# Kernel optimization log

Hardware: AMD Instinct MI355X
Metric: run time of the kernel (lower is better)

The kernel has to match this reference:

```python
import jax, jax.numpy as jnp
import numpy as np

N_EMBD = 2048
N_HEAD = 32
N_KV_HEADS = 8
HEAD_DIM = 64
N_REP = N_HEAD // N_KV_HEADS
MAX_SEQ_LEN = 4096
ROPE_THETA = 10000.0


def _precompute_freqs_cis(dim, end, theta=ROPE_THETA):
    freqs = 1.0 / theta ** (jnp.arange(0, dim, 2)[: dim // 2].astype(jnp.float32) / dim)
    t = jnp.arange(end, dtype=jnp.float32)
    freqs = jnp.outer(t, freqs)  # (end, dim//2)
    return jnp.cos(freqs), jnp.sin(freqs)


def setup_inputs() -> dict:
    key = jax.random.key(0)
    ks = jax.random.split(key, 5)
    B, S = 2, 2048
    x = jax.random.normal(ks[0], (B, S, N_EMBD), dtype=jnp.float32)
    # torch Linear(in, out, bias=False): y = x @ W.T, W is (out, in). We store (in, out).
    sc = 1.0 / np.sqrt(N_EMBD)
    wq = jax.random.normal(ks[1], (N_EMBD, N_EMBD), dtype=jnp.float32) * sc
    wk = jax.random.normal(ks[2], (N_EMBD, N_KV_HEADS * HEAD_DIM), dtype=jnp.float32) * sc
    wv = jax.random.normal(ks[3], (N_EMBD, N_KV_HEADS * HEAD_DIM), dtype=jnp.float32) * sc
    wo = jax.random.normal(ks[4], (N_EMBD, N_EMBD), dtype=jnp.float32) * sc
    freqs_cos, freqs_sin = _precompute_freqs_cis(HEAD_DIM, MAX_SEQ_LEN)
    return {"x": x, "wq": wq, "wk": wk, "wv": wv, "wo": wo,
            "freqs_cos": freqs_cos, "freqs_sin": freqs_sin}


def _apply_rotary(t, cos, sin):
    # t: (B, S, H, HD); interleaved real/imag pairs along last dim.
    shp = t.shape
    t2 = t.reshape(*shp[:-1], HEAD_DIM // 2, 2)
    r, i = t2[..., 0], t2[..., 1]
    out_r = r * cos - i * sin
    out_i = r * sin + i * cos
    return jnp.stack([out_r, out_i], axis=-1).reshape(shp)


def reference(x, wq, wk, wv, wo, freqs_cos, freqs_sin):
    B, S, _ = x.shape
    xq = (x @ wq).reshape(B, S, N_HEAD, HEAD_DIM)
    xk = (x @ wk).reshape(B, S, N_KV_HEADS, HEAD_DIM)
    xv = (x @ wv).reshape(B, S, N_KV_HEADS, HEAD_DIM)

    cos = freqs_cos[:S][None, :, None, :]  # (1, S, 1, HD/2)
    sin = freqs_sin[:S][None, :, None, :]
    xq = _apply_rotary(xq, cos, sin)
    xk = _apply_rotary(xk, cos, sin)

    # GQA: repeat KV heads (repeat_interleave along head dim)
    keys = jnp.repeat(xk, N_REP, axis=2)    # (B, S, H, HD)
    values = jnp.repeat(xv, N_REP, axis=2)

    scores = jnp.einsum('bqhd,bkhd->bhqk', xq, keys) / np.sqrt(HEAD_DIM)
    causal = jnp.tril(jnp.ones((S, S), dtype=bool))
    scores = jnp.where(causal, scores, -jnp.inf)
    probs = jax.nn.softmax(scores.astype(jnp.float32), axis=-1).astype(xq.dtype)
    out = jnp.einsum('bhqk,bkhd->bqhd', probs, values)  # (B, S, H, HD)
    out = out.reshape(B, S, N_EMBD)
    return out @ wo
```

## Files before the change

### kernel.cpp

```cpp
#include <hip/hip_runtime.h>
#include <hip/hip_fp16.h>
#include <stdint.h>

typedef _Float16 f16x8 __attribute__((ext_vector_type(8)));
typedef _Float16 f16x4 __attribute__((ext_vector_type(4)));
typedef _Float16 f16x2 __attribute__((ext_vector_type(2)));
typedef float f32x4 __attribute__((ext_vector_type(4)));
typedef float f32x16 __attribute__((ext_vector_type(16)));

#define B_ 2
#define S_ 2048
#define NE 2048
#define NH 32
#define NKV 8
#define HD 64
#define NTOK (B_ * S_)
#define QKVN 3072

__device__ __forceinline__ f16x2 pk(float a, float b) {
  return __builtin_bit_cast(f16x2, __builtin_amdgcn_cvt_pkrtz(a, b));
}

__device__ __forceinline__ void gld_lds16(void* lds, const void* g) {
  __builtin_amdgcn_global_load_lds(
      (const __attribute__((address_space(1))) void*)g,
      (__attribute__((address_space(3))) void*)lds, 16, 0, 0);
}

__global__ void conv_x_kernel(const float* __restrict__ x,
                              _Float16* __restrict__ xo, int n2) {
  int i = blockIdx.x * 256 + threadIdx.x;
  if (i < n2) {
    float2 v = ((const float2*)x)[i];
    f16x2 h;
    h.x = (_Float16)v.x;
    h.y = (_Float16)v.y;
    ((f16x2*)xo)[i] = h;
  }
}

__global__ void tconv_kernel(const float* __restrict__ src,
                             _Float16* __restrict__ dst,
                             int srcN, int rowoff, int ldd) {
  __shared__ float tile[32][33];
  int n0 = blockIdx.x * 32, k0 = blockIdx.y * 32;
  int tx = threadIdx.x, ty = threadIdx.y;
  for (int i = ty; i < 32; i += 8)
    tile[i][tx] = src[(size_t)(k0 + i) * srcN + n0 + tx];
  __syncthreads();
  for (int i = ty; i < 32; i += 8)
    dst[(size_t)(rowoff + n0 + i) * ldd + k0 + tx] = (_Float16)tile[tx][i];
}

template <int OUT_F32>
__global__ __launch_bounds__(256, 2) void gemm_bt(
    const _Float16* __restrict__ A, const _Float16* __restrict__ Bt,
    void* __restrict__ Cout, int M, int N, int K) {
  __shared__ _Float16 As[128 * 32];
  __shared__ _Float16 Bs[128 * 32];
  const int tid = threadIdx.x;
  const int wave = tid >> 6, lane = tid & 63;
  const int qd = lane >> 4, ln = lane & 15;
  const int m0 = blockIdx.y * 128, n0 = blockIdx.x * 128;
  const int wm = (wave >> 1) * 64, wn = (wave & 1) * 64;

  f32x4 acc[4][4] = {};

  const int srow = (lane >> 2);
  const int scol = (lane & 3) * 8;

  for (int k0 = 0; k0 < K; k0 += 32) {
    __syncthreads();
#pragma unroll
    for (int it = 0; it < 2; ++it) {
      int r = wave * 32 + it * 16 + srow;
      gld_lds16(&As[(wave * 32 + it * 16) * 32],
                A + (size_t)(m0 + r) * K + k0 + scol);
      gld_lds16(&Bs[(wave * 32 + it * 16) * 32],
                Bt + (size_t)(n0 + r) * K + k0 + scol);
    }
    __syncthreads();
    f16x8 a[4], b[4];
#pragma unroll
    for (int mt = 0; mt < 4; ++mt)
      a[mt] = *(const f16x8*)&As[(wm + mt * 16 + ln) * 32 + qd * 8];
#pragma unroll
    for (int nt = 0; nt < 4; ++nt)
      b[nt] = *(const f16x8*)&Bs[(wn + nt * 16 + ln) * 32 + qd * 8];
#pragma unroll
    for (int mt = 0; mt < 4; ++mt)
#pragma unroll
      for (int nt = 0; nt < 4; ++nt)
        acc[mt][nt] =
            __builtin_amdgcn_mfma_f32_16x16x32_f16(a[mt], b[nt], acc[mt][nt], 0, 0, 0);
  }

#pragma unroll
  for (int mt = 0; mt < 4; ++mt) {
    int row = m0 + wm + mt * 16 + qd * 4;
#pragma unroll
    for (int nt = 0; nt < 4; ++nt) {
      int col = n0 + wn + nt * 16 + ln;
#pragma unroll
      for (int r = 0; r < 4; ++r) {
        if (OUT_F32)
          ((float*)Cout)[(size_t)(row + r) * N + col] = acc[mt][nt][r];
        else
          ((_Float16*)Cout)[(size_t)(row + r) * N + col] =
              (_Float16)acc[mt][nt][r];
      }
    }
  }
}

__global__ void rope_scatter_kernel(const _Float16* __restrict__ qkv,
                                    const float* __restrict__ fcos,
                                    const float* __restrict__ fsin,
                                    _Float16* __restrict__ Qb,
                                    _Float16* __restrict__ Kb) {
  const float QSC = 0.125f * 1.44269504088896f;
  int idx = blockIdx.x * 256 + threadIdx.x;
  int t = idx / 1280;
  int col = (idx - t * 1280) * 2;
  int b = t >> 11, s = t & 2047;
  float v0 = (float)qkv[(size_t)t * QKVN + col];
  float v1 = (float)qkv[(size_t)t * QKVN + col + 1];
  _Float16* dst;
  size_t off;
  int d;
  float sc;
  if (col < 2048) {
    int h = col >> 6;
    d = col & 63;
    dst = Qb;
    off = ((size_t)(b * NH + h) * S_ + s) * HD + d;
    sc = QSC;
  } else {
    int cc = col - 2048;
    int h = cc >> 6;
    d = cc & 63;
    dst = Kb;
    off = ((size_t)(b * NKV + h) * S_ + s) * HD + d;
    sc = 1.0f;
  }
  float c = fcos[s * 32 + (d >> 1)], sn = fsin[s * 32 + (d >> 1)];
  f16x2 o;
  o.x = (_Float16)((v0 * c - v1 * sn) * sc);
  o.y = (_Float16)((v0 * sn + v1 * c) * sc);
  *(f16x2*)(dst + off) = o;
}

__global__ void vtrans_kernel(const _Float16* __restrict__ qkv,
                              _Float16* __restrict__ Vtg) {
  __shared__ _Float16 tile[64][65];
  int t0 = blockIdx.x * 64;
  int kv = blockIdx.y, b = blockIdx.z;
  int tid = threadIdx.x;
  for (int slot = tid; slot < 4096; slot += 256) {
    int r = slot >> 6, c = slot & 63;
    tile[r][c] = qkv[(size_t)(b * S_ + t0 + r) * QKVN + 2560 + kv * 64 + c];
  }
  __syncthreads();
  size_t base = ((size_t)(b * NKV + kv) * HD) * S_;
  for (int slot = tid; slot < 4096; slot += 256) {
    int d = slot >> 6, r = slot & 63;
    Vtg[base + (size_t)d * S_ + t0 + r] = tile[r][d];
  }
}

__global__ __launch_bounds__(128, 2) void attn_kernel(
    const _Float16* __restrict__ Qb, const _Float16* __restrict__ Kb,
    const _Float16* __restrict__ Vtg, _Float16* __restrict__ Ob) {
  constexpr float M_SHIFT = 10.0f;
  __shared__ _Float16 Ks[64 * 64];
  __shared__ _Float16 Vs[64 * 64];
  const int tid = threadIdx.x;
  const int wave = tid >> 6, lane = tid & 63;
  const int mrow = lane & 31;
  const bool half = (lane >> 5) != 0;
  const int h = blockIdx.y, b = blockIdx.z;
  const int kvh = h >> 2;

  const _Float16* Qh = Qb + ((size_t)(b * NH + h) * S_) * HD;
  const _Float16* Kh = Kb + ((size_t)(b * NKV + kvh) * S_) * HD;
  const _Float16* Vh = Vtg + ((size_t)(b * NKV + kvh) * HD) * S_;

  const int sr = tid >> 3;
  const int scc = tid & 7;
  const int swz = (scc ^ (sr & 7)) * 8;

#pragma unroll
  for (int pass = 0; pass < 2; ++pass) {
    const int qt = pass ? blockIdx.x : (31 - blockIdx.x);
    const int q0 = qt * 64;
    const int nkt = qt + 1;

    const int qrow = q0 + wave * 32 + mrow;
    f16x8 aq[4];
#pragma unroll
    for (int kk = 0; kk < 4; ++kk)
      aq[kk] = *(const f16x8*)(Qh + (size_t)qrow * HD + kk * 16 +
                               (half ? 8 : 0));

    f32x16 accO[2] = {};
    float lsum = 0.f;

    f16x8 kp[4], vp[4];
#pragma unroll
    for (int i = 0; i < 4; ++i) {
      kp[i] = *(const f16x8*)(Kh + (size_t)(sr + i * 16) * HD + scc * 8);
      vp[i] = *(const f16x8*)(Vh + (size_t)(sr + i * 16) * S_ + scc * 8);
    }
#pragma unroll
    for (int i = 0; i < 4; ++i) {
      *(f16x8*)&Ks[(sr + i * 16) * 64 + swz] = kp[i];
      *(f16x8*)&Vs[(sr + i * 16) * 64 + swz] = vp[i];
    }

    for (int kt = 0; kt < nkt; ++kt) {
      __syncthreads();
      if (kt + 1 < nkt) {
#pragma unroll
        for (int i = 0; i < 4; ++i) {
          kp[i] = *(const f16x8*)(Kh +
                                  (size_t)((kt + 1) * 64 + sr + i * 16) * HD +
                                  scc * 8);
          vp[i] = *(const f16x8*)(Vh + (size_t)(sr + i * 16) * S_ +
                                  (kt + 1) * 64 + scc * 8);
        }
      }

      f32x16 s[2];
#pragma unroll
      for (int nt = 0; nt < 2; ++nt)
#pragma unroll
        for (int r = 0; r < 16; ++r) s[nt][r] = -M_SHIFT;
#pragma unroll
      for (int kk = 0; kk < 4; ++kk) {
        int c = kk * 2 + (half ? 1 : 0);
#pragma unroll
        for (int nt = 0; nt < 2; ++nt) {
          int krow = nt * 32 + mrow;
          f16x8 bk = *(const f16x8*)&Ks[krow * 64 + ((c ^ (krow & 7)) * 8)];
          s[nt] = __builtin_amdgcn_mfma_f32_32x32x16_f16(bk, aq[kk], s[nt],
                                                         0, 0, 0);
        }
      }

      const bool edge = (kt == nkt - 1);
      float pf[2][16];
#pragma unroll
      for (int nt = 0; nt < 2; ++nt)
#pragma unroll
        for (int r = 0; r < 16; ++r) {
          int key = kt * 64 + nt * 32 + (r & 3) + 8 * (r >> 2) +
                    (half ? 4 : 0);
          float p = exp2f(s[nt][r]);
          if (edge && key > qrow) p = 0.f;
          lsum += p;
          pf[nt][r] = p;
        }

      f16x2 P2[2][4][2];
#pragma unroll
      for (int nt = 0; nt < 2; ++nt)
#pragma unroll
        for (int c = 0; c < 4; ++c)
#pragma unroll
          for (int u = 0; u < 2; ++u)
            P2[nt][c][u] = pk(pf[nt][4 * c + 2 * u], pf[nt][4 * c + 2 * u + 1]);

#pragma unroll
      for (int s4 = 0; s4 < 4; ++s4) {
        const int ntp = s4 >> 1;
        const int gA = (2 * s4) & 3, gB = (2 * s4 + 1) & 3;
        f16x2 own0 = half ? P2[ntp][gB][0] : P2[ntp][gA][0];
        f16x2 own1 = half ? P2[ntp][gB][1] : P2[ntp][gA][1];
        f16x2 snd0 = half ? P2[ntp][gA][0] : P2[ntp][gB][0];
        f16x2 snd1 = half ? P2[ntp][gA][1] : P2[ntp][gB][1];
        f16x2 rcv0 = __builtin_bit_cast(
            f16x2, __shfl_xor(__builtin_bit_cast(int, snd0), 32));
        f16x2 rcv1 = __builtin_bit_cast(
            f16x2, __shfl_xor(__builtin_bit_cast(int, snd1), 32));
        union {
          f16x2 h2[4];
          f16x8 h8;
        } bp;
        bp.h2[0] = half ? rcv0 : own0;
        bp.h2[1] = half ? rcv1 : own1;
        bp.h2[2] = half ? own0 : rcv0;
        bp.h2[3] = half ? own1 : rcv1;
        const int c = 2 * s4 + (half ? 1 : 0);
#pragma unroll
        for (int ntd = 0; ntd < 2; ++ntd) {
          int drow = ntd * 32 + mrow;
          f16x8 bv = *(const f16x8*)&Vs[drow * 64 + ((c ^ (drow & 7)) * 8)];
          accO[ntd] = __builtin_amdgcn_mfma_f32_32x32x16_f16(bv, bp.h8,
                                                             accO[ntd], 0, 0, 0);
        }
      }

      __syncthreads();
      if (kt + 1 < nkt) {
#pragma unroll
        for (int i = 0; i < 4; ++i) {
          *(f16x8*)&Ks[(sr + i * 16) * 64 + swz] = kp[i];
          *(f16x8*)&Vs[(sr + i * 16) * 64 + swz] = vp[i];
        }
      }
    }

    float tot = lsum + __shfl_xor(lsum, 32);
    float inv = 1.f / tot;
    size_t base = ((size_t)(b * S_) + qrow) * NE + h * HD;
#pragma unroll
    for (int ntd = 0; ntd < 2; ++ntd)
#pragma unroll
      for (int rq = 0; rq < 4; ++rq) {
        int d0 = ntd * 32 + 8 * rq + (half ? 4 : 0);
        union {
          f16x2 h2[2];
          f16x4 h4;
        } o;
        o.h2[0] = pk(accO[ntd][4 * rq + 0] * inv, accO[ntd][4 * rq + 1] * inv);
        o.h2[1] = pk(accO[ntd][4 * rq + 2] * inv, accO[ntd][4 * rq + 3] * inv);
        *(f16x4*)(Ob + base + d0) = o.h4;
      }
  }
}

extern "C" void kernel_launch(void* const* d_in, const int* in_sizes, int n_in,
                              void* d_out, int out_size, void* d_ws,
                              size_t ws_size, hipStream_t stream) {
  const float* x = (const float*)d_in[0];
  const float* wq = (const float*)d_in[1];
  const float* wk = (const float*)d_in[2];
  const float* wv = (const float*)d_in[3];
  const float* wo = (const float*)d_in[4];
  const float* fcos = (const float*)d_in[5];
  const float* fsin = (const float*)d_in[6];

  char* ws = (char*)d_ws;
  _Float16* xb = (_Float16*)(ws);
  _Float16* wqkv_t = (_Float16*)(ws + 16777216);
  _Float16* wo_t = (_Float16*)(ws + 29360128);
  _Float16* qkv = (_Float16*)(ws + 37748736);
  _Float16* Qb = (_Float16*)(ws + 62914560);
  _Float16* Kb = (_Float16*)(ws + 79691776);
  _Float16* Vb = (_Float16*)(ws + 83886080);
  _Float16* Ob = (_Float16*)(ws + 88080384);

  conv_x_kernel<<<16384, 256, 0, stream>>>(x, xb, (NTOK * NE) / 2);

  dim3 tb(32, 8);
  tconv_kernel<<<dim3(64, 64), tb, 0, stream>>>(wq, wqkv_t, 2048, 0, 2048);
  tconv_kernel<<<dim3(16, 64), tb, 0, stream>>>(wk, wqkv_t, 512, 2048, 2048);
  tconv_kernel<<<dim3(16, 64), tb, 0, stream>>>(wv, wqkv_t, 512, 2560, 2048);
  tconv_kernel<<<dim3(64, 64), tb, 0, stream>>>(wo, wo_t, 2048, 0, 2048);

  gemm_bt<0><<<dim3(QKVN / 128, NTOK / 128), 256, 0, stream>>>(
      xb, wqkv_t, qkv, NTOK, QKVN, NE);

  rope_scatter_kernel<<<(NTOK * 1280) / 256, 256, 0, stream>>>(qkv, fcos, fsin,
                                                               Qb, Kb);
  vtrans_kernel<<<dim3(S_ / 64, NKV, B_), 256, 0, stream>>>(qkv, Vb);

  attn_kernel<<<dim3(16, NH, B_), 128, 0, stream>>>(Qb, Kb, Vb, Ob);

  gemm_bt<1><<<dim3(NE / 128, NTOK / 128), 256, 0, stream>>>(
      Ob, wo_t, d_out, NTOK, NE, NE);
}
```

Measured before the change: 327.2 us.

## Split attention KV loop across two wave pairs and reduce partials in LDS

The attention block grows from 2 to 4 waves. Each pair of waves processes alternate KV tiles using its own K/V LDS buffers, so each pair covers about half the key range for the same 64 query rows. The partial output accumulators and row sums from pair 1 are passed through LDS and added into pair 0, which then normalises and writes the result. This doubles the waves available per query tile to hide latency on the causal loop. In exchange it costs extra LDS, a final cross-pair reduction, and some redundant tile loads when a pair has no valid tile.

```diff
diff --git a/kernel.cpp b/kernel.cpp
--- a/kernel.cpp
+++ b/kernel.cpp
@@ -168,25 +168,33 @@
   }
 }
 
-__global__ __launch_bounds__(128, 2) void attn_kernel(
+__global__ __launch_bounds__(256, 4) void attn_kernel(
     const _Float16* __restrict__ Qb, const _Float16* __restrict__ Kb,
     const _Float16* __restrict__ Vtg, _Float16* __restrict__ Ob) {
   constexpr float M_SHIFT = 10.0f;
-  __shared__ _Float16 Ks[64 * 64];
-  __shared__ _Float16 Vs[64 * 64];
+  __shared__ _Float16 smem[4 * 64 * 64];
+  __shared__ float lsx[128];
   const int tid = threadIdx.x;
-  const int wave = tid >> 6, lane = tid & 63;
+  const int wave = tid >> 6;
+  const int pair = wave >> 1;
+  const int wq = wave & 1;
+  const int lane = tid & 63;
   const int mrow = lane & 31;
   const bool half = (lane >> 5) != 0;
   const int h = blockIdx.y, b = blockIdx.z;
   const int kvh = h >> 2;
 
+  _Float16* Ksp = smem + pair * 8192;
+  _Float16* Vsp = Ksp + 4096;
+  float* cb = (float*)smem;
+
   const _Float16* Qh = Qb + ((size_t)(b * NH + h) * S_) * HD;
   const _Float16* Kh = Kb + ((size_t)(b * NKV + kvh) * S_) * HD;
   const _Float16* Vh = Vtg + ((size_t)(b * NKV + kvh) * HD) * S_;
 
-  const int sr = tid >> 3;
-  const int scc = tid & 7;
+  const int ptid = tid & 127;
+  const int sr = ptid >> 3;
+  const int scc = ptid & 7;
   const int swz = (scc ^ (sr & 7)) * 8;
 
 #pragma unroll
@@ -194,8 +202,9 @@
     const int qt = pass ? blockIdx.x : (31 - blockIdx.x);
     const int q0 = qt * 64;
     const int nkt = qt + 1;
-
-    const int qrow = q0 + wave * 32 + mrow;
+    const int NI = (nkt + 1) >> 1;
+
+    const int qrow = q0 + wq * 32 + mrow;
     f16x8 aq[4];
 #pragma unroll
     for (int kk = 0; kk < 4; ++kk)
@@ -205,127 +214,159 @@
     f32x16 accO[2] = {};
     float lsum = 0.f;
 
+    const int t0 = (pair < nkt) ? pair : (nkt - 1);
     f16x8 kp[4], vp[4];
 #pragma unroll
     for (int i = 0; i < 4; ++i) {
-      kp[i] = *(const f16x8*)(Kh + (size_t)(sr + i * 16) * HD + scc * 8);
-      vp[i] = *(const f16x8*)(Vh + (size_t)(sr + i * 16) * S_ + scc * 8);
+      kp[i] = *(const f16x8*)(Kh + (size_t)(t0 * 64 + sr + i * 16) * HD +
+                              scc * 8);
+      vp[i] = *(const f16x8*)(Vh + (size_t)(sr + i * 16) * S_ + t0 * 64 +
+                              scc * 8);
     }
 #pragma unroll
     for (int i = 0; i < 4; ++i) {
-      *(f16x8*)&Ks[(sr + i * 16) * 64 + swz] = kp[i];
-      *(f16x8*)&Vs[(sr + i * 16) * 64 + swz] = vp[i];
-    }
-
-    for (int kt = 0; kt < nkt; ++kt) {
+      *(f16x8*)&Ksp[(sr + i * 16) * 64 + swz] = kp[i];
+      *(f16x8*)&Vsp[(sr + i * 16) * 64 + swz] = vp[i];
+    }
+
+    for (int it = 0; it < NI; ++it) {
       __syncthreads();
-      if (kt + 1 < nkt) {
+      const int kt = 2 * it + pair;
+      const bool valid = kt < nkt;
+      if (it + 1 < NI) {
+        const int tn0 = 2 * (it + 1) + pair;
+        const int tn = (tn0 < nkt) ? tn0 : (nkt - 1);
 #pragma unroll
         for (int i = 0; i < 4; ++i) {
-          kp[i] = *(const f16x8*)(Kh +
-                                  (size_t)((kt + 1) * 64 + sr + i * 16) * HD +
+          kp[i] = *(const f16x8*)(Kh + (size_t)(tn * 64 + sr + i * 16) * HD +
                                   scc * 8);
-          vp[i] = *(const f16x8*)(Vh + (size_t)(sr + i * 16) * S_ +
-                                  (kt + 1) * 64 + scc * 8);
+          vp[i] = *(const f16x8*)(Vh + (size_t)(sr + i * 16) * S_ + tn * 64 +
+                                  scc * 8);
         }
       }
 
-      f32x16 s[2];
-#pragma unroll
-      for (int nt = 0; nt < 2; ++nt)
-#pragma unroll
-        for (int r = 0; r < 16; ++r) s[nt][r] = -M_SHIFT;
-#pragma unroll
-      for (int kk = 0; kk < 4; ++kk) {
-        int c = kk * 2 + (half ? 1 : 0);
-#pragma unroll
-        for (int nt = 0; nt < 2; ++nt) {
-          int krow = nt * 32 + mrow;
-          f16x8 bk = *(const f16x8*)&Ks[krow * 64 + ((c ^ (krow & 7)) * 8)];
-          s[nt] = __builtin_amdgcn_mfma_f32_32x32x16_f16(bk, aq[kk], s[nt],
-                                                         0, 0, 0);
+      if (valid) {
+        f32x16 s[2];
+#pragma unroll
+        for (int nt = 0; nt < 2; ++nt)
+#pragma unroll
+          for (int r = 0; r < 16; ++r) s[nt][r] = -M_SHIFT;
+#pragma unroll
+        for (int kk = 0; kk < 4; ++kk) {
+          int c = kk * 2 + (half ? 1 : 0);
+#pragma unroll
+          for (int nt = 0; nt < 2; ++nt) {
+            int krow = nt * 32 + mrow;
+            f16x8 bk = *(const f16x8*)&Ksp[krow * 64 + ((c ^ (krow & 7)) * 8)];
+            s[nt] = __builtin_amdgcn_mfma_f32_32x32x16_f16(bk, aq[kk], s[nt],
+                                                           0, 0, 0);
+          }
+        }
+
+        const bool edge = (kt == nkt - 1);
+        float pf[2][16];
+#pragma unroll
+        for (int nt = 0; nt < 2; ++nt)
+#pragma unroll
+          for (int r = 0; r < 16; ++r) {
+            int key = kt * 64 + nt * 32 + (r & 3) + 8 * (r >> 2) +
+                      (half ? 4 : 0);
+            float p = exp2f(s[nt][r]);
+            if (edge && key > qrow) p = 0.f;
+            lsum += p;
+            pf[nt][r] = p;
+          }
+
+        f16x2 P2[2][4][2];
+#pragma unroll
+        for (int nt = 0; nt < 2; ++nt)
+#pragma unroll
+          for (int c = 0; c < 4; ++c)
+#pragma unroll
+            for (int u = 0; u < 2; ++u)
+              P2[nt][c][u] =
+                  pk(pf[nt][4 * c + 2 * u], pf[nt][4 * c + 2 * u + 1]);
+
+#pragma unroll
+        for (int s4 = 0; s4 < 4; ++s4) {
+          const int ntp = s4 >> 1;
+          const int gA = (2 * s4) & 3, gB = (2 * s4 + 1) & 3;
+          f16x2 own0 = half ? P2[ntp][gB][0] : P2[ntp][gA][0];
+          f16x2 own1 = half ? P2[ntp][gB][1] : P2[ntp][gA][1];
+          f16x2 snd0 = half ? P2[ntp][gA][0] : P2[ntp][gB][0];
+          f16x2 snd1 = half ? P2[ntp][gA][1] : P2[ntp][gB][1];
+          f16x2 rcv0 = __builtin_bit_cast(
+              f16x2, __shfl_xor(__builtin_bit_cast(int, snd0), 32));
+          f16x2 rcv1 = __builtin_bit_cast(
+              f16x2, __shfl_xor(__builtin_bit_cast(int, snd1), 32));
+          union {
+            f16x2 h2[4];
+            f16x8 h8;
+          } bp;
+          bp.h2[0] = half ? rcv0 : own0;
+          bp.h2[1] = half ? rcv1 : own1;
+          bp.h2[2] = half ? own0 : rcv0;
+          bp.h2[3] = half ? own1 : rcv1;
+          const int c = 2 * s4 + (half ? 1 : 0);
+#pragma unroll
+          for (int ntd = 0; ntd < 2; ++ntd) {
+            int drow = ntd * 32 + mrow;
+            f16x8 bv = *(const f16x8*)&Vsp[drow * 64 + ((c ^ (drow & 7)) * 8)];
+            accO[ntd] = __builtin_amdgcn_mfma_f32_32x32x16_f16(
+                bv, bp.h8, accO[ntd], 0, 0, 0);
+          }
         }
       }
 
-      const bool edge = (kt == nkt - 1);
-      float pf[2][16];
-#pragma unroll
-      for (int nt = 0; nt < 2; ++nt)
-#pragma unroll
-        for (int r = 0; r < 16; ++r) {
-          int key = kt * 64 + nt * 32 + (r & 3) + 8 * (r >> 2) +
-                    (half ? 4 : 0);
-          float p = exp2f(s[nt][r]);
-          if (edge && key > qrow) p = 0.f;
-          lsum += p;
-          pf[nt][r] = p;
-        }
-
-      f16x2 P2[2][4][2];
-#pragma unroll
-      for (int nt = 0; nt < 2; ++nt)
-#pragma unroll
-        for (int c = 0; c < 4; ++c)
-#pragma unroll
-          for (int u = 0; u < 2; ++u)
-            P2[nt][c][u] = pk(pf[nt][4 * c + 2 * u], pf[nt][4 * c + 2 * u + 1]);
-
-#pragma unroll
-      for (int s4 = 0; s4 < 4; ++s4) {
-        const int ntp = s4 >> 1;
-        const int gA = (2 * s4) & 3, gB = (2 * s4 + 1) & 3;
-        f16x2 own0 = half ? P2[ntp][gB][0] : P2[ntp][gA][0];
-        f16x2 own1 = half ? P2[ntp][gB][1] : P2[ntp][gA][1];
-        f16x2 snd0 = half ? P2[ntp][gA][0] : P2[ntp][gB][0];
-        f16x2 snd1 = half ? P2[ntp][gA][1] : P2[ntp][gB][1];
-        f16x2 rcv0 = __builtin_bit_cast(
-            f16x2, __shfl_xor(__builtin_bit_cast(int, snd0), 32));
-        f16x2 rcv1 = __builtin_bit_cast(
-            f16x2, __shfl_xor(__builtin_bit_cast(int, snd1), 32));
-        union {
-          f16x2 h2[4];
-          f16x8 h8;
-        } bp;
-        bp.h2[0] = half ? rcv0 : own0;
-        bp.h2[1] = half ? rcv1 : own1;
-        bp.h2[2] = half ? own0 : rcv0;
-        bp.h2[3] = half ? own1 : rcv1;
-        const int c = 2 * s4 + (half ? 1 : 0);
-#pragma unroll
-        for (int ntd = 0; ntd < 2; ++ntd) {
-          int drow = ntd * 32 + mrow;
-          f16x8 bv = *(const f16x8*)&Vs[drow * 64 + ((c ^ (drow & 7)) * 8)];
-          accO[ntd] = __builtin_amdgcn_mfma_f32_32x32x16_f16(bv, bp.h8,
-                                                             accO[ntd], 0, 0, 0);
+      __syncthreads();
+      if (it + 1 < NI) {
+#pragma unroll
+        for (int i = 0; i < 4; ++i) {
+          *(f16x8*)&Ksp[(sr + i * 16) * 64 + swz] = kp[i];
+          *(f16x8*)&Vsp[(sr + i * 16) * 64 + swz] = vp[i];
         }
       }
-
-      __syncthreads();
-      if (kt + 1 < nkt) {
-#pragma unroll
-        for (int i = 0; i < 4; ++i) {
-          *(f16x8*)&Ks[(sr + i * 16) * 64 + swz] = kp[i];
-          *(f16x8*)&Vs[(sr + i * 16) * 64 + swz] = vp[i];
+    }
+
+    if (pair == 1) {
+      float* my = cb + (wq * 64 + lane) * 33;
+#pragma unroll
+      for (int nt = 0; nt < 2; ++nt)
+#pragma unroll
+        for (int r = 0; r < 16; ++r) my[nt * 16 + r] = accO[nt][r];
+      lsx[wq * 64 + lane] = lsum;
+    }
+    __syncthreads();
+    if (pair == 0) {
+      const float* my = cb + (wq * 64 + lane) * 33;
+#pragma unroll
+      for (int nt = 0; nt < 2; ++nt)
+#pragma unroll
+        for (int r = 0; r < 16; ++r) accO[nt][r] += my[nt * 16 + r];
+      lsum += lsx[wq * 64 + lane];
+    }
+    __syncthreads();
+
+    if (pair == 0) {
+      float tot = lsum + __shfl_xor(lsum, 32);
+      float inv = 1.f / tot;
+      size_t base = ((size_t)(b * S_) + qrow) * NE + h * HD;
+#pragma unroll
+      for (int ntd = 0; ntd < 2; ++ntd)
+#pragma unroll
+        for (int rq = 0; rq < 4; ++rq) {
+          int d0 = ntd * 32 + 8 * rq + (half ? 4 : 0);
+          union {
+            f16x2 h2[2];
+            f16x4 h4;
+          } o;
+          o.h2[0] =
+              pk(accO[ntd][4 * rq + 0] * inv, accO[ntd][4 * rq + 1] * inv);
+          o.h2[1] =
+              pk(accO[ntd][4 * rq + 2] * inv, accO[ntd][4 * rq + 3] * inv);
+          *(f16x4*)(Ob + base + d0) = o.h4;
         }
-      }
-    }
-
-    float tot = lsum + __shfl_xor(lsum, 32);
-    float inv = 1.f / tot;
-    size_t base = ((size_t)(b * S_) + qrow) * NE + h * HD;
-#pragma unroll
-    for (int ntd = 0; ntd < 2; ++ntd)
-#pragma unroll
-      for (int rq = 0; rq < 4; ++rq) {
-        int d0 = ntd * 32 + 8 * rq + (half ? 4 : 0);
-        union {
-          f16x2 h2[2];
-          f16x4 h4;
-        } o;
-        o.h2[0] = pk(accO[ntd][4 * rq + 0] * inv, accO[ntd][4 * rq + 1] * inv);
-        o.h2[1] = pk(accO[ntd][4 * rq + 2] * inv, accO[ntd][4 * rq + 3] * inv);
-        *(f16x4*)(Ob + base + d0) = o.h4;
-      }
+    }
   }
 }
 
@@ -365,7 +406,7 @@
                                                                Qb, Kb);
   vtrans_kernel<<<dim3(S_ / 64, NKV, B_), 256, 0, stream>>>(qkv, Vb);
 
-  attn_kernel<<<dim3(16, NH, B_), 128, 0, stream>>>(Qb, Kb, Vb, Ob);
+  attn_kernel<<<dim3(16, NH, B_), 256, 0, stream>>>(Qb, Kb, Vb, Ob);
 
   gemm_bt<1><<<dim3(NE / 128, NTOK / 128), 256, 0, stream>>>(
       Ob, wo_t, d_out, NTOK, NE, NE);
```

Result: slower. 378.2 us (+15.6%).
